# Optimization experiments

Hardware: AMD Instinct MI355X
Metric: run time of the kernel (lower is better)

The kernel has to match this reference:

```python
import jax, jax.numpy as jnp
import numpy as np
from jax import lax

S, B = 2048, 2048          # seq_len, batch (seq-first layout like nn.LSTM)
IN, H, OUT, L = 2, 4, 1, 4  # from module defaults


def setup_inputs() -> dict:
    key = jax.random.key(0)
    ks = jax.random.split(key, 11)
    s = 0.5  # ~ PyTorch init scale 1/sqrt(H)
    return {
        "x": jax.random.normal(ks[0], (S, B, IN), jnp.float32),
        "W_ih0": jax.random.normal(ks[1], (4 * H, IN), jnp.float32) * s,
        "W_hh0": jax.random.normal(ks[2], (4 * H, H), jnp.float32) * s,
        "b_ih0": jax.random.normal(ks[3], (4 * H,), jnp.float32) * s,
        "b_hh0": jax.random.normal(ks[4], (4 * H,), jnp.float32) * s,
        "W_ihr": jax.random.normal(ks[5], (L - 1, 4 * H, H), jnp.float32) * s,
        "W_hhr": jax.random.normal(ks[6], (L - 1, 4 * H, H), jnp.float32) * s,
        "b_ihr": jax.random.normal(ks[7], (L - 1, 4 * H), jnp.float32) * s,
        "b_hhr": jax.random.normal(ks[8], (L - 1, 4 * H), jnp.float32) * s,
        "W_out": jax.random.normal(ks[9], (OUT, H), jnp.float32) * s,
        "b_out": jax.random.normal(ks[10], (OUT,), jnp.float32) * s,
    }


def _lstm_layer(x, Wih, Whh, b):
    # x: [S, B, D_in]; PyTorch gate order: i, f, g, o
    Bsz = x.shape[1]
    Hh = Whh.shape[1]
    # precompute input contribution for all timesteps (batched GEMM)
    xg = jnp.einsum('sbd,gd->sbg', x, Wih) + b  # [S, B, 4H]

    def step(carry, xgt):
        h, c = carry
        gates = xgt + h @ Whh.T  # [B, 4H]
        i, f, g, o = jnp.split(gates, 4, axis=-1)
        c = jax.nn.sigmoid(f) * c + jax.nn.sigmoid(i) * jnp.tanh(g)
        h = jax.nn.sigmoid(o) * jnp.tanh(c)
        return (h, c), h

    init = (jnp.zeros((Bsz, Hh), x.dtype), jnp.zeros((Bsz, Hh), x.dtype))
    _, ys = lax.scan(step, init, xg)
    return ys  # [S, B, H]


def reference(x, W_ih0, W_hh0, b_ih0, b_hh0, W_ihr, W_hhr, b_ihr, b_hhr, W_out, b_out):
    h = _lstm_layer(x, W_ih0, W_hh0, b_ih0 + b_hh0)
    for l in range(W_ihr.shape[0]):  # fixed small layer loop
        h = _lstm_layer(h, W_ihr[l], W_hhr[l], b_ihr[l] + b_hhr[l])
    # dropout: identity in eval mode (deterministic reference)
    y = jnp.einsum('sbh,oh->sbo', h, W_out) + b_out  # linear head, [S, B, 1]
    return y
```

## Files before the change

kernel.cpp:

```cpp
#include <hip/hip_runtime.h>

#define S_LEN 2048
#define B_SZ 2048

typedef float v2 __attribute__((ext_vector_type(2)));
#define FMA2(a, b, c) __builtin_elementwise_fma((a), (b), (c))

template <int CTRL>
__device__ __forceinline__ float dppmov(float v) {
  int r = __builtin_amdgcn_update_dpp(0, __builtin_bit_cast(int, v), CTRL, 0xF,
                                      0xF, true);
  return __builtin_bit_cast(float, r);
}

template <int CTRL, bool BC>
__device__ __forceinline__ float dppold(float old, float v) {
  int r = __builtin_amdgcn_update_dpp(__builtin_bit_cast(int, old),
                                      __builtin_bit_cast(int, v), CTRL, 0xF,
                                      0xF, BC);
  return __builtin_bit_cast(float, r);
}

#define TICK(U)                                                                \
  {                                                                            \
            \
    float ns0 = dppold<0x114, false>(xc##U.x, hv01.x);          \
    float ns1 = dppold<0x114, false>(xc##U.y, hv01.y);                         \
    float ns2 = dppold<0x114, true>(0.0f, hv23.x);                             \
    float ns3 = dppold<0x114, true>(0.0f, hv23.y);                             \
    v2 h01, h23;                                                               \
    h01.x = hx0;                                                               \
    h01.y = hx1;                                                               \
    h23.x = hx2;                                                               \
    h23.y = hx3;                                                               \
    v2 A0 = FMA2(wi01[0], h01, bias2[0]);                                      \
    v2 A1 = FMA2(wi01[1], h01, bias2[1]);                                      \
    v2 A2 = FMA2(wi01[2], h01, bias2[2]);                                      \
    v2 A3 = FMA2(wi01[3], h01, bias2[3]);                                      \
    A0 = FMA2(wi23[0], h23, A0);                                               \
    A1 = FMA2(wi23[1], h23, A1);                                               \
    A2 = FMA2(wi23[2], h23, A2);                                               \
    A3 = FMA2(wi23[3], h23, A3);                                               \
    A0 = FMA2(wh01[0], hv01, A0);                                              \
    A1 = FMA2(wh01[1], hv01, A1);                                              \
    A2 = FMA2(wh01[2], hv01, A2);                                              \
    A3 = FMA2(wh01[3], hv01, A3);                                              \
    A0 = FMA2(wh23[0], hv23, A0);                                              \
    A1 = FMA2(wh23[1], hv23, A1);                                              \
    A2 = FMA2(wh23[2], hv23, A2);                                              \
    A3 = FMA2(wh23[3], hv23, A3);                                              \
    float a0 = A0.x + A0.y, a1 = A1.x + A1.y;                                  \
    float a2 = A2.x + A2.y, a3 = A3.x + A3.y;                                  \
    float e0 = __builtin_amdgcn_exp2f(a0);       \
    float e1 = __builtin_amdgcn_exp2f(a1);                                     \
    float e2 = __builtin_amdgcn_exp2f(a2);                                     \
    float e3 = __builtin_amdgcn_exp2f(a3);                                     \
    float r0 = __builtin_amdgcn_rcpf(1.0f + e0);               \
    float r1 = __builtin_amdgcn_rcpf(1.0f + e1);               \
    float r2 = __builtin_amdgcn_rcpf(1.0f + e2);            \
    float r3 = __builtin_amdgcn_rcpf(1.0f + e3);               \
    float gi = KT * r0;                               \
    float gg = fmaf(2.0f, r2, -1.0f);                             \
    cKT = fmaf(r1, cKT, gi * gg);                                              \
    float te = __builtin_amdgcn_exp2f(cKT);                                    \
    float tr = __builtin_amdgcn_rcpf(1.0f + te);                               \
    float go2 = r3 + r3;                                                       \
    float hh = fmaf(go2, tr, -r3);                          \
    hv01.x = hh;                                                               \
    hv01.y = dppmov<0x39>(hh);                                \
    hv23.x = dppmov<0x4E>(hh);                                \
    hv23.y = dppmov<0x93>(hh);                                \
             \
    y##U = FMA2(wo01v, hv01, bo2);                                             \
    y##U = FMA2(wo23v, hv23, y##U);                                            \
    hx0 = ns0;                                                                 \
    hx1 = ns1;                                                                 \
    hx2 = ns2;                                                                 \
    hx3 = ns3;                                                                 \
  }

#define RESET(U)                                                               \
  if (2 * l > (U)) {                                                           \
    cKT = 0.0f;                                                                \
    hv01.x = 0.0f;                                                             \
    hv01.y = 0.0f;                                                             \
    hv23.x = 0.0f;                                                             \
    hv23.y = 0.0f;                                                             \
  }

#define XLOAD(U) xc##U = pxk[(U)*B_SZ];
#define XLOAD7C xc7 = pxk[6 * B_SZ];

#define YST(U) ypk[(U)*B_SZ] = y##U.x + y##U.y;

__global__ void __launch_bounds__(64, 1)
    lstm_kernel(const float *__restrict__ x, const float *__restrict__ Wih0,
                const float *__restrict__ Whh0, const float *__restrict__ bih0,
                const float *__restrict__ bhh0, const float *__restrict__ Wihr,
                const float *__restrict__ Whhr, const float *__restrict__ bihr,
                const float *__restrict__ bhhr, const float *__restrict__ Wout,
                const float *__restrict__ bout, float *__restrict__ out) {
  const int lane = threadIdx.x & 63;
  const int b = lane >> 4;
  const int l = (lane >> 2) & 3;
  const int j = lane & 3;
  const int bidx = blockIdx.x * 4 + b;
  const bool lz = (l == 0);
  const bool yl = (l == 3) && (j == 0);

  const float L2E = 1.4426950408889634f;
  const float KT = -2.8853900817779268f;
  const float kks[4] = {-L2E, -L2E, -2.0f * L2E, -L2E};

  v2 wi01[4], wi23[4], wh01[4], wh23[4], bias2[4];
#pragma unroll
  for (int t = 0; t < 4; ++t) {
    const int row = t * 4 + j;
    const float kk = kks[t];
    float i0, i1, i2, i3, w0, w1, w2, w3, bs;
    if (l == 0) {
      i0 = Wih0[row * 2 + 0];
      i1 = Wih0[row * 2 + 1];
      i2 = 0.0f;
      i3 = 0.0f;
      w0 = Whh0[row * 4 + j];
      w1 = Whh0[row * 4 + ((j + 1) & 3)];
      w2 = Whh0[row * 4 + ((j + 2) & 3)];
      w3 = Whh0[row * 4 + ((j + 3) & 3)];
      bs = bih0[row] + bhh0[row];
    } else {
      const int m = l - 1;
      i0 = Wihr[m * 64 + row * 4 + j];
      i1 = Wihr[m * 64 + row * 4 + ((j + 1) & 3)];
      i2 = Wihr[m * 64 + row * 4 + ((j + 2) & 3)];
      i3 = Wihr[m * 64 + row * 4 + ((j + 3) & 3)];
      w0 = Whhr[m * 64 + row * 4 + j];
      w1 = Whhr[m * 64 + row * 4 + ((j + 1) & 3)];
      w2 = Whhr[m * 64 + row * 4 + ((j + 2) & 3)];
      w3 = Whhr[m * 64 + row * 4 + ((j + 3) & 3)];
      bs = bihr[m * 16 + row] + bhhr[m * 16 + row];
    }
    wi01[t].x = kk * i0;
    wi01[t].y = kk * i1;
    wi23[t].x = kk * i2;
    wi23[t].y = kk * i3;
    wh01[t].x = kk * w0;
    wh01[t].y = kk * w1;
    wh23[t].x = kk * w2;
    wh23[t].y = kk * w3;
    bias2[t].x = kk * bs;
    bias2[t].y = 0.0f;
  }
  v2 wo01v, wo23v, bo2;
  wo01v.x = Wout[0];
  wo01v.y = Wout[1];
  wo23v.x = Wout[2];
  wo23v.y = Wout[3];
  bo2.x = bout[0];
  bo2.y = 0.0f;

  const float2 *__restrict__ px = (const float2 *)x;

  v2 hv01, hv23;
  hv01.x = 0.0f;
  hv01.y = 0.0f;
  hv23.x = 0.0f;
  hv23.y = 0.0f;
  float cKT = 0.0f;
  float hx0, hx1, hx2, hx3;
  v2 y0, y1, y2, y3, y4, y5, y6, y7;

  {
    float2 x00 = px[bidx];
    hx0 = lz ? x00.x : 0.0f;
    hx1 = lz ? x00.y : 0.0f;
    hx2 = 0.0f;
    hx3 = 0.0f;
  }

  float2 xc0 = px[1 * B_SZ + bidx];
  float2 xc1 = px[2 * B_SZ + bidx];
  float2 xc2 = px[3 * B_SZ + bidx];
  float2 xc3 = px[4 * B_SZ + bidx];
  float2 xc4 = px[5 * B_SZ + bidx];
  float2 xc5 = px[6 * B_SZ + bidx];
  float2 xc6 = px[7 * B_SZ + bidx];
  float2 xc7 = px[8 * B_SZ + bidx];

  const float2 *__restrict__ pxk = px + 9 * B_SZ + bidx;
  float *__restrict__ ypk;

  TICK(0); RESET(0); XLOAD(0);
  TICK(1); RESET(1); XLOAD(1);
  TICK(2); RESET(2); XLOAD(2);
  TICK(3); RESET(3); XLOAD(3);
  TICK(4); RESET(4); XLOAD(4);
  TICK(5); RESET(5); XLOAD(5);
  TICK(6); XLOAD(6);
  TICK(7); XLOAD(7);
  if (yl) {
    out[bidx] = y6.x + y6.y;
    out[B_SZ + bidx] = y7.x + y7.y;
  }
  pxk += 8 * B_SZ;
  ypk = out + 2 * B_SZ + bidx;

#pragma unroll 1
  for (int k = 1; k < 254; ++k) {
    TICK(0); XLOAD(0);
    TICK(1); XLOAD(1);
    TICK(2); XLOAD(2);
    TICK(3); XLOAD(3);
    TICK(4); XLOAD(4);
    TICK(5); XLOAD(5);
    TICK(6); XLOAD(6);
    TICK(7); XLOAD(7);
    if (yl) {
      YST(0); YST(1); YST(2); YST(3); YST(4); YST(5); YST(6); YST(7);
    }
    pxk += 8 * B_SZ;
    ypk += 8 * B_SZ;
  }

  TICK(0); XLOAD(0);
  TICK(1); XLOAD(1);
  TICK(2); XLOAD(2);
  TICK(3); XLOAD(3);
  TICK(4); XLOAD(4);
  TICK(5); XLOAD(5);
  TICK(6); XLOAD(6);
  TICK(7); XLOAD7C;
  if (yl) {
    YST(0); YST(1); YST(2); YST(3); YST(4); YST(5); YST(6); YST(7);
  }
  ypk += 8 * B_SZ;

  TICK(0);
  TICK(1);
  TICK(2);
  TICK(3);
  TICK(4);
  TICK(5);
  TICK(6);
  TICK(7);
  if (yl) {
    YST(0); YST(1); YST(2); YST(3); YST(4); YST(5); YST(6); YST(7);
  }
  ypk += 8 * B_SZ;

  TICK(0);
  TICK(1);
  TICK(2);
  TICK(3);
  TICK(4);
  TICK(5);
  if (yl) {
    YST(0); YST(1); YST(2); YST(3); YST(4); YST(5);
  }
}

extern "C" void kernel_launch(void *const *d_in, const int *in_sizes, int n_in,
                              void *d_out, int out_size, void *d_ws,
                              size_t ws_size, hipStream_t stream) {
  (void)in_sizes;
  (void)n_in;
  (void)out_size;
  (void)d_ws;
  (void)ws_size;
  const float *x = (const float *)d_in[0];
  const float *Wih0 = (const float *)d_in[1];
  const float *Whh0 = (const float *)d_in[2];
  const float *bih0 = (const float *)d_in[3];
  const float *bhh0 = (const float *)d_in[4];
  const float *Wihr = (const float *)d_in[5];
  const float *Whhr = (const float *)d_in[6];
  const float *bihr = (const float *)d_in[7];
  const float *bhhr = (const float *)d_in[8];
  const float *Wout = (const float *)d_in[9];
  const float *bout = (const float *)d_in[10];
  lstm_kernel<<<dim3(B_SZ / 4), dim3(64), 0, stream>>>(
      x, Wih0, Whh0, bih0, bhh0, Wihr, Whhr, bihr, bhhr, Wout, bout,
      (float *)d_out);
}
```

Baseline: 366.4 us.

## Interleave two independent batch groups per wavefront for ILP in LSTM recurrence

Each wavefront now advances two independent sets of four batch elements (A and B) through the layer-wavefront LSTM pipeline, interleaving their FMA, transcendental and DPP chains. The grid shrinks from 512 to 256 single-wave blocks. The aim is to hide the long serial dependency latency of each recurrent step with independent work, at the cost of more registers and fewer wavefronts in flight across the 256 CUs.

```diff
diff --git a/kernel.cpp b/kernel.cpp
--- a/kernel.cpp
+++ b/kernel.cpp
@@ -21,77 +21,129 @@
   return __builtin_bit_cast(float, r);
 }
 
-#define TICK(U)                                                                \
+#define TICK2(U)                                                               \
   {                                                                            \
-            \
-    float ns0 = dppold<0x114, false>(xc##U.x, hv01.x);          \
-    float ns1 = dppold<0x114, false>(xc##U.y, hv01.y);                         \
-    float ns2 = dppold<0x114, true>(0.0f, hv23.x);                             \
-    float ns3 = dppold<0x114, true>(0.0f, hv23.y);                             \
-    v2 h01, h23;                                                               \
-    h01.x = hx0;                                                               \
-    h01.y = hx1;                                                               \
-    h23.x = hx2;                                                               \
-    h23.y = hx3;                                                               \
-    v2 A0 = FMA2(wi01[0], h01, bias2[0]);                                      \
-    v2 A1 = FMA2(wi01[1], h01, bias2[1]);                                      \
-    v2 A2 = FMA2(wi01[2], h01, bias2[2]);                                      \
-    v2 A3 = FMA2(wi01[3], h01, bias2[3]);                                      \
-    A0 = FMA2(wi23[0], h23, A0);                                               \
-    A1 = FMA2(wi23[1], h23, A1);                                               \
-    A2 = FMA2(wi23[2], h23, A2);                                               \
-    A3 = FMA2(wi23[3], h23, A3);                                               \
-    A0 = FMA2(wh01[0], hv01, A0);                                              \
-    A1 = FMA2(wh01[1], hv01, A1);                                              \
-    A2 = FMA2(wh01[2], hv01, A2);                                              \
-    A3 = FMA2(wh01[3], hv01, A3);                                              \
-    A0 = FMA2(wh23[0], hv23, A0);                                              \
-    A1 = FMA2(wh23[1], hv23, A1);                                              \
-    A2 = FMA2(wh23[2], hv23, A2);                                              \
-    A3 = FMA2(wh23[3], hv23, A3);                                              \
-    float a0 = A0.x + A0.y, a1 = A1.x + A1.y;                                  \
-    float a2 = A2.x + A2.y, a3 = A3.x + A3.y;                                  \
-    float e0 = __builtin_amdgcn_exp2f(a0);       \
-    float e1 = __builtin_amdgcn_exp2f(a1);                                     \
-    float e2 = __builtin_amdgcn_exp2f(a2);                                     \
-    float e3 = __builtin_amdgcn_exp2f(a3);                                     \
-    float r0 = __builtin_amdgcn_rcpf(1.0f + e0);               \
-    float r1 = __builtin_amdgcn_rcpf(1.0f + e1);               \
-    float r2 = __builtin_amdgcn_rcpf(1.0f + e2);            \
-    float r3 = __builtin_amdgcn_rcpf(1.0f + e3);               \
-    float gi = KT * r0;                               \
-    float gg = fmaf(2.0f, r2, -1.0f);                             \
-    cKT = fmaf(r1, cKT, gi * gg);                                              \
-    float te = __builtin_amdgcn_exp2f(cKT);                                    \
-    float tr = __builtin_amdgcn_rcpf(1.0f + te);                               \
-    float go2 = r3 + r3;                                                       \
-    float hh = fmaf(go2, tr, -r3);                          \
-    hv01.x = hh;                                                               \
-    hv01.y = dppmov<0x39>(hh);                                \
-    hv23.x = dppmov<0x4E>(hh);                                \
-    hv23.y = dppmov<0x93>(hh);                                \
+    v2 h01A, h23A, h01B, h23B;                                                 \
+    h01A.x = hx0_A;                                                            \
+    h01B.x = hx0_B;                                                            \
+    h01A.y = hx1_A;                                                            \
+    h01B.y = hx1_B;                                                            \
+    h23A.x = hx2_A;                                                            \
+    h23B.x = hx2_B;                                                            \
+    h23A.y = hx3_A;                                                            \
+    h23B.y = hx3_B;                                                            \
+    v2 A0 = FMA2(wi01[0], h01A, bias2[0]);                                     \
+    v2 B0 = FMA2(wi01[0], h01B, bias2[0]);                                     \
+    v2 A1 = FMA2(wi01[1], h01A, bias2[1]);                                     \
+    v2 B1 = FMA2(wi01[1], h01B, bias2[1]);                                     \
+    v2 A2 = FMA2(wi01[2], h01A, bias2[2]);                                     \
+    v2 B2 = FMA2(wi01[2], h01B, bias2[2]);                                     \
+    v2 A3 = FMA2(wi01[3], h01A, bias2[3]);                                     \
+    v2 B3 = FMA2(wi01[3], h01B, bias2[3]);                                     \
+    A0 = FMA2(wi23[0], h23A, A0);                                              \
+    B0 = FMA2(wi23[0], h23B, B0);                                              \
+    A1 = FMA2(wi23[1], h23A, A1);                                              \
+    B1 = FMA2(wi23[1], h23B, B1);                                              \
+    A2 = FMA2(wi23[2], h23A, A2);                                              \
+    B2 = FMA2(wi23[2], h23B, B2);                                              \
+    A3 = FMA2(wi23[3], h23A, A3);                                              \
+    B3 = FMA2(wi23[3], h23B, B3);                                              \
+    A0 = FMA2(wh01[0], hv01_A, A0);                                            \
+    B0 = FMA2(wh01[0], hv01_B, B0);                                            \
+    A1 = FMA2(wh01[1], hv01_A, A1);                                            \
+    B1 = FMA2(wh01[1], hv01_B, B1);                                            \
+    A2 = FMA2(wh01[2], hv01_A, A2);                                            \
+    B2 = FMA2(wh01[2], hv01_B, B2);                                            \
+    A3 = FMA2(wh01[3], hv01_A, A3);                                            \
+    B3 = FMA2(wh01[3], hv01_B, B3);                                            \
+    A0 = FMA2(wh23[0], hv23_A, A0);                                            \
+    B0 = FMA2(wh23[0], hv23_B, B0);                                            \
+    A1 = FMA2(wh23[1], hv23_A, A1);                                            \
+    B1 = FMA2(wh23[1], hv23_B, B1);                                            \
+    A2 = FMA2(wh23[2], hv23_A, A2);                                            \
+    B2 = FMA2(wh23[2], hv23_B, B2);                                            \
+    A3 = FMA2(wh23[3], hv23_A, A3);                                            \
+    B3 = FMA2(wh23[3], hv23_B, B3);                                            \
+    float a0A = A0.x + A0.y, a0B = B0.x + B0.y;                                \
+    float a1A = A1.x + A1.y, a1B = B1.x + B1.y;                                \
+    float a2A = A2.x + A2.y, a2B = B2.x + B2.y;                                \
+    float a3A = A3.x + A3.y, a3B = B3.x + B3.y;                                \
+    float e0A = __builtin_amdgcn_exp2f(a0A);                                   \
+    float e0B = __builtin_amdgcn_exp2f(a0B);                                   \
+    float e1A = __builtin_amdgcn_exp2f(a1A);                                   \
+    float e1B = __builtin_amdgcn_exp2f(a1B);                                   \
+    float e2A = __builtin_amdgcn_exp2f(a2A);                                   \
+    float e2B = __builtin_amdgcn_exp2f(a2B);                                   \
+    float e3A = __builtin_amdgcn_exp2f(a3A);                                   \
+    float e3B = __builtin_amdgcn_exp2f(a3B);                                   \
+    float r0A = __builtin_amdgcn_rcpf(1.0f + e0A);             \
+    float r0B = __builtin_amdgcn_rcpf(1.0f + e0B);                             \
+    float r1A = __builtin_amdgcn_rcpf(1.0f + e1A);             \
+    float r1B = __builtin_amdgcn_rcpf(1.0f + e1B);                             \
+    float r2A = __builtin_amdgcn_rcpf(1.0f + e2A);          \
+    float r2B = __builtin_amdgcn_rcpf(1.0f + e2B);                             \
+    float r3A = __builtin_amdgcn_rcpf(1.0f + e3A);             \
+    float r3B = __builtin_amdgcn_rcpf(1.0f + e3B);                             \
+    float giA = KT * r0A, giB = KT * r0B;             \
+    float ggA = fmaf(2.0f, r2A, -1.0f);                           \
+    float ggB = fmaf(2.0f, r2B, -1.0f);                                        \
+    cKT_A = fmaf(r1A, cKT_A, giA * ggA);                                       \
+    cKT_B = fmaf(r1B, cKT_B, giB * ggB);                                       \
+    float teA = __builtin_amdgcn_exp2f(cKT_A);                                 \
+    float teB = __builtin_amdgcn_exp2f(cKT_B);                                 \
+    float trA = __builtin_amdgcn_rcpf(1.0f + teA);                             \
+    float trB = __builtin_amdgcn_rcpf(1.0f + teB);                             \
+    float go2A = r3A + r3A, go2B = r3B + r3B;                                  \
+    float hhA = fmaf(go2A, trA, -r3A);                      \
+    float hhB = fmaf(go2B, trB, -r3B);                                         \
+         \
+    hx0_A = dppold<0x114, false>(xc##U##_A.x, hv01_A.x);        \
+    hx0_B = dppold<0x114, false>(xc##U##_B.x, hv01_B.x);                       \
+    hx1_A = dppold<0x114, false>(xc##U##_A.y, hv01_A.y);                       \
+    hx1_B = dppold<0x114, false>(xc##U##_B.y, hv01_B.y);                       \
+    hx2_A = dppold<0x114, true>(0.0f, hv23_A.x);                               \
+    hx2_B = dppold<0x114, true>(0.0f, hv23_B.x);                               \
+    hx3_A = dppold<0x114, true>(0.0f, hv23_A.y);                               \
+    hx3_B = dppold<0x114, true>(0.0f, hv23_B.y);                               \
+    hv01_A.x = hhA;                                                            \
+    hv01_B.x = hhB;                                                            \
+    hv01_A.y = dppmov<0x39>(hhA);                             \
+    hv01_B.y = dppmov<0x39>(hhB);                                              \
+    hv23_A.x = dppmov<0x4E>(hhA);                             \
+    hv23_B.x = dppmov<0x4E>(hhB);                                              \
+    hv23_A.y = dppmov<0x93>(hhA);                             \
+    hv23_B.y = dppmov<0x93>(hhB);                                              \
              \
-    y##U = FMA2(wo01v, hv01, bo2);                                             \
-    y##U = FMA2(wo23v, hv23, y##U);                                            \
-    hx0 = ns0;                                                                 \
-    hx1 = ns1;                                                                 \
-    hx2 = ns2;                                                                 \
-    hx3 = ns3;                                                                 \
-  }
-
-#define RESET(U)                                                               \
+    y##U##_A = FMA2(wo01v, hv01_A, bo2);                                       \
+    y##U##_B = FMA2(wo01v, hv01_B, bo2);                                       \
+    y##U##_A = FMA2(wo23v, hv23_A, y##U##_A);                                  \
+    y##U##_B = FMA2(wo23v, hv23_B, y##U##_B);                                  \
+  }
+
+#define RESET2(U)                                                              \
   if (2 * l > (U)) {                                                           \
-    cKT = 0.0f;                                                                \
-    hv01.x = 0.0f;                                                             \
-    hv01.y = 0.0f;                                                             \
-    hv23.x = 0.0f;                                                             \
-    hv23.y = 0.0f;                                                             \
-  }
-
-#define XLOAD(U) xc##U = pxk[(U)*B_SZ];
-#define XLOAD7C xc7 = pxk[6 * B_SZ];
-
-#define YST(U) ypk[(U)*B_SZ] = y##U.x + y##U.y;
+    cKT_A = 0.0f;                                                              \
+    cKT_B = 0.0f;                                                              \
+    hv01_A.x = 0.0f;                                                           \
+    hv01_A.y = 0.0f;                                                           \
+    hv23_A.x = 0.0f;                                                           \
+    hv23_A.y = 0.0f;                                                           \
+    hv01_B.x = 0.0f;                                                           \
+    hv01_B.y = 0.0f;                                                           \
+    hv23_B.x = 0.0f;                                                           \
+    hv23_B.y = 0.0f;                                                           \
+  }
+
+#define XLOAD2(U)                                                              \
+  xc##U##_A = pxk[(U)*B_SZ];                                                   \
+  xc##U##_B = pxk[(U)*B_SZ + 4];
+#define XLOAD7C2                                                               \
+  xc7_A = pxk[6 * B_SZ];                          \
+  xc7_B = pxk[6 * B_SZ + 4];
+
+#define YST2(U)                                                                \
+  ypk[(U)*B_SZ] = y##U##_A.x + y##U##_A.y;                                     \
+  ypk[(U)*B_SZ + 4] = y##U##_B.x + y##U##_B.y;
 
 __global__ void __launch_bounds__(64, 1)
     lstm_kernel(const float *__restrict__ x, const float *__restrict__ Wih0,
@@ -104,7 +156,7 @@
   const int b = lane >> 4;
   const int l = (lane >> 2) & 3;
   const int j = lane & 3;
-  const int bidx = blockIdx.x * 4 + b;
+  const int bidxA = blockIdx.x * 8 + b;
   const bool lz = (l == 0);
   const bool yl = (l == 3) && (j == 0);
 
@@ -161,101 +213,111 @@
 
   const float2 *__restrict__ px = (const float2 *)x;
 
-  v2 hv01, hv23;
-  hv01.x = 0.0f;
-  hv01.y = 0.0f;
-  hv23.x = 0.0f;
-  hv23.y = 0.0f;
-  float cKT = 0.0f;
-  float hx0, hx1, hx2, hx3;
-  v2 y0, y1, y2, y3, y4, y5, y6, y7;
+  v2 hv01_A, hv23_A, hv01_B, hv23_B;
+  hv01_A.x = 0.0f; hv01_A.y = 0.0f; hv23_A.x = 0.0f; hv23_A.y = 0.0f;
+  hv01_B.x = 0.0f; hv01_B.y = 0.0f; hv23_B.x = 0.0f; hv23_B.y = 0.0f;
+  float cKT_A = 0.0f, cKT_B = 0.0f;
+  float hx0_A, hx1_A, hx2_A, hx3_A;
+  float hx0_B, hx1_B, hx2_B, hx3_B;
+  v2 y0_A, y1_A, y2_A, y3_A, y4_A, y5_A, y6_A, y7_A;
+  v2 y0_B, y1_B, y2_B, y3_B, y4_B, y5_B, y6_B, y7_B;
 
   {
-    float2 x00 = px[bidx];
-    hx0 = lz ? x00.x : 0.0f;
-    hx1 = lz ? x00.y : 0.0f;
-    hx2 = 0.0f;
-    hx3 = 0.0f;
-  }
-
-  float2 xc0 = px[1 * B_SZ + bidx];
-  float2 xc1 = px[2 * B_SZ + bidx];
-  float2 xc2 = px[3 * B_SZ + bidx];
-  float2 xc3 = px[4 * B_SZ + bidx];
-  float2 xc4 = px[5 * B_SZ + bidx];
-  float2 xc5 = px[6 * B_SZ + bidx];
-  float2 xc6 = px[7 * B_SZ + bidx];
-  float2 xc7 = px[8 * B_SZ + bidx];
-
-  const float2 *__restrict__ pxk = px + 9 * B_SZ + bidx;
+    float2 xA = px[bidxA];
+    float2 xB = px[bidxA + 4];
+    hx0_A = lz ? xA.x : 0.0f;
+    hx1_A = lz ? xA.y : 0.0f;
+    hx0_B = lz ? xB.x : 0.0f;
+    hx1_B = lz ? xB.y : 0.0f;
+    hx2_A = 0.0f;
+    hx3_A = 0.0f;
+    hx2_B = 0.0f;
+    hx3_B = 0.0f;
+  }
+
+  float2 xc0_A = px[1 * B_SZ + bidxA], xc0_B = px[1 * B_SZ + bidxA + 4];
+  float2 xc1_A = px[2 * B_SZ + bidxA], xc1_B = px[2 * B_SZ + bidxA + 4];
+  float2 xc2_A = px[3 * B_SZ + bidxA], xc2_B = px[3 * B_SZ + bidxA + 4];
+  float2 xc3_A = px[4 * B_SZ + bidxA], xc3_B = px[4 * B_SZ + bidxA + 4];
+  float2 xc4_A = px[5 * B_SZ + bidxA], xc4_B = px[5 * B_SZ + bidxA + 4];
+  float2 xc5_A = px[6 * B_SZ + bidxA], xc5_B = px[6 * B_SZ + bidxA + 4];
+  float2 xc6_A = px[7 * B_SZ + bidxA], xc6_B = px[7 * B_SZ + bidxA + 4];
+  float2 xc7_A = px[8 * B_SZ + bidxA], xc7_B = px[8 * B_SZ + bidxA + 4];
+
+  const float2 *__restrict__ pxk = px + 9 * B_SZ + bidxA;
   float *__restrict__ ypk;
 
-  TICK(0); RESET(0); XLOAD(0);
-  TICK(1); RESET(1); XLOAD(1);
-  TICK(2); RESET(2); XLOAD(2);
-  TICK(3); RESET(3); XLOAD(3);
-  TICK(4); RESET(4); XLOAD(4);
-  TICK(5); RESET(5); XLOAD(5);
-  TICK(6); XLOAD(6);
-  TICK(7); XLOAD(7);
+  TICK2(0); RESET2(0); XLOAD2(0);
+  TICK2(1); RESET2(1); XLOAD2(1);
+  TICK2(2); RESET2(2); XLOAD2(2);
+  TICK2(3); RESET2(3); XLOAD2(3);
+  TICK2(4); RESET2(4); XLOAD2(4);
+  TICK2(5); RESET2(5); XLOAD2(5);
+  TICK2(6); XLOAD2(6);
+  TICK2(7); XLOAD2(7);
   if (yl) {
-    out[bidx] = y6.x + y6.y;
-    out[B_SZ + bidx] = y7.x + y7.y;
+    out[bidxA] = y6_A.x + y6_A.y;
+    out[bidxA + 4] = y6_B.x + y6_B.y;
+    out[B_SZ + bidxA] = y7_A.x + y7_A.y;
+    out[B_SZ + bidxA + 4] = y7_B.x + y7_B.y;
   }
   pxk += 8 * B_SZ;
-  ypk = out + 2 * B_SZ + bidx;
+  ypk = out + 2 * B_SZ + bidxA;
 
 #pragma unroll 1
   for (int k = 1; k < 254; ++k) {
-    TICK(0); XLOAD(0);
-    TICK(1); XLOAD(1);
-    TICK(2); XLOAD(2);
-    TICK(3); XLOAD(3);
-    TICK(4); XLOAD(4);
-    TICK(5); XLOAD(5);
-    TICK(6); XLOAD(6);
-    TICK(7); XLOAD(7);
+    TICK2(0); XLOAD2(0);
+    TICK2(1); XLOAD2(1);
+    TICK2(2); XLOAD2(2);
+    TICK2(3); XLOAD2(3);
+    TICK2(4); XLOAD2(4);
+    TICK2(5); XLOAD2(5);
+    TICK2(6); XLOAD2(6);
+    TICK2(7); XLOAD2(7);
     if (yl) {
-      YST(0); YST(1); YST(2); YST(3); YST(4); YST(5); YST(6); YST(7);
+      YST2(0); YST2(1); YST2(2); YST2(3);
+      YST2(4); YST2(5); YST2(6); YST2(7);
     }
     pxk += 8 * B_SZ;
     ypk += 8 * B_SZ;
   }
 
-  TICK(0); XLOAD(0);
-  TICK(1); XLOAD(1);
-  TICK(2); XLOAD(2);
-  TICK(3); XLOAD(3);
-  TICK(4); XLOAD(4);
-  TICK(5); XLOAD(5);
-  TICK(6); XLOAD(6);
-  TICK(7); XLOAD7C;
+  TICK2(0); XLOAD2(0);
+  TICK2(1); XLOAD2(1);
+  TICK2(2); XLOAD2(2);
+  TICK2(3); XLOAD2(3);
+  TICK2(4); XLOAD2(4);
+  TICK2(5); XLOAD2(5);
+  TICK2(6); XLOAD2(6);
+  TICK2(7); XLOAD7C2;
   if (yl) {
-    YST(0); YST(1); YST(2); YST(3); YST(4); YST(5); YST(6); YST(7);
+    YST2(0); YST2(1); YST2(2); YST2(3);
+    YST2(4); YST2(5); YST2(6); YST2(7);
   }
   ypk += 8 * B_SZ;
 
-  TICK(0);
-  TICK(1);
-  TICK(2);
-  TICK(3);
-  TICK(4);
-  TICK(5);
-  TICK(6);
-  TICK(7);
+  TICK2(0);
+  TICK2(1);
+  TICK2(2);
+  TICK2(3);
+  TICK2(4);
+  TICK2(5);
+  TICK2(6);
+  TICK2(7);
   if (yl) {
-    YST(0); YST(1); YST(2); YST(3); YST(4); YST(5); YST(6); YST(7);
+    YST2(0); YST2(1); YST2(2); YST2(3);
+    YST2(4); YST2(5); YST2(6); YST2(7);
   }
   ypk += 8 * B_SZ;
 
-  TICK(0);
-  TICK(1);
-  TICK(2);
-  TICK(3);
-  TICK(4);
-  TICK(5);
+  TICK2(0);
+  TICK2(1);
+  TICK2(2);
+  TICK2(3);
+  TICK2(4);
+  TICK2(5);
   if (yl) {
-    YST(0); YST(1); YST(2); YST(3); YST(4); YST(5);
+    YST2(0); YST2(1); YST2(2); YST2(3); YST2(4); YST2(5);
   }
 }
 
@@ -278,7 +340,7 @@
   const float *bhhr = (const float *)d_in[8];
   const float *Wout = (const float *)d_in[9];
   const float *bout = (const float *)d_in[10];
-  lstm_kernel<<<dim3(B_SZ / 4), dim3(64), 0, stream>>>(
+  lstm_kernel<<<dim3(B_SZ / 8), dim3(64), 0, stream>>>(
       x, Wih0, Whh0, bih0, bhh0, Wihr, Whhr, bihr, bhhr, Wout, bout,
       (float *)d_out);
 }
```

Result: slower. 574.7 us (+56.8%).
